# Performance work log

Measured on AMD Instinct MI355X. Metric: run time of the kernel, lower is better.

Reference implementation:

```python
import jax, jax.numpy as jnp
import numpy as np

DIM = 768
HEADS = 12
FRAMES = 16
T = FRAMES // 2          # temporal length per stream = 8
N = 196                  # spatial patch tokens (14x14)
B = 16                   # batch
SCALE = (DIM // HEADS) ** -0.5


def setup_inputs() -> dict:
    key = jax.random.key(0)
    ks = jax.random.split(key, 10)
    return {
        "s_x": jax.random.normal(ks[0], (N + 1, B * T, DIM), jnp.float32),
        "t_x": jax.random.normal(ks[1], (B, T * N, DIM), jnp.float32),
        "clip_time_pos": SCALE * jax.random.normal(ks[2], (T, DIM), jnp.float32),
        "vmae_time_pos": SCALE * jax.random.normal(ks[3], (T, DIM), jnp.float32),
        "Wq": jax.random.normal(ks[4], (DIM, DIM), jnp.float32) * 0.02,
        "q_bias": jnp.zeros((DIM,), jnp.float32),
        "Wkv": jax.random.normal(ks[5], (2 * DIM, DIM), jnp.float32) * 0.02,
        "kv_bias": jnp.zeros((2 * DIM,), jnp.float32),
        "Wproj": jax.random.normal(ks[6], (DIM, DIM), jnp.float32) * 0.02,
        "proj_bias": jnp.zeros((DIM,), jnp.float32),
    }


def reference(s_x, t_x, clip_time_pos, vmae_time_pos,
              Wq, q_bias, Wkv, kv_bias, Wproj, proj_bias):
    b = t_x.shape[0]
    t = s_x.shape[1] // b            # = FRAMES // 2
    n = s_x.shape[0] - 1             # spatial tokens (CLS excluded)
    d = s_x.shape[-1]
    h = HEADS
    hd = d // h
    scale = hd ** -0.5

    s_cls = s_x[0]                                   # [b*t, d]
    # 'n (b t) d -> (b n) t d'
    s_pat = s_x[1:].reshape(n, b, t, d).transpose(1, 0, 2, 3).reshape(b * n, t, d)
    s_pat = s_pat + clip_time_pos                    # [(b n), t, d]
    # 'b (t n) d -> (b n) t d'
    tx = t_x.reshape(b, t, n, d).transpose(0, 2, 1, 3).reshape(b * n, t, d)
    tx = tx + vmae_time_pos

    # projections (bias added manually as in F.linear with explicit bias)
    q = (s_pat @ Wq.T + q_bias).reshape(b * n, t, h, hd).transpose(0, 2, 1, 3)  # [bn,h,t,hd]
    kv = (tx @ Wkv.T + kv_bias).reshape(b * n, t, 2, h, hd)                      # e outermost in (e h d)
    k = kv[:, :, 0].transpose(0, 2, 1, 3)            # [bn,h,t,hd]
    v = kv[:, :, 1].transpose(0, 2, 1, 3)

    attn = jax.nn.softmax(jnp.einsum('bhqd,bhkd->bhqk', q * scale, k), axis=-1)
    out = jnp.einsum('bhqk,bhkd->bhqd', attn, v)     # [bn,h,t,hd]
    out = out.transpose(0, 2, 1, 3).reshape(b * n, t, d)
    out = out @ Wproj.T + proj_bias
    # '(b n) t d -> n (b t) d'
    out = out.reshape(b, n, t, d).transpose(1, 0, 2, 3).reshape(n, b * t, d)
    return jnp.concatenate([s_cls[None], out], axis=0)
```

## Files before the change

### kernel.cpp

```cpp
#include <hip/hip_runtime.h>
#include <stdint.h>

#define DIM   768
#define NTOK  196
#define TT    8
#define MROWS 25088
#define HEADS 12
#define NKT   12

typedef __bf16 bf16x8 __attribute__((ext_vector_type(8)));
typedef float  f32x4  __attribute__((ext_vector_type(4)));
typedef unsigned short u16x4 __attribute__((ext_vector_type(4)));
typedef unsigned short u16x8 __attribute__((ext_vector_type(8)));

typedef __attribute__((address_space(1))) const void GAS;
typedef __attribute__((address_space(3))) void LAS;

__device__ inline unsigned short f2bf(float f) {
  uint32_t u = __builtin_bit_cast(uint32_t, f);
  u += 0x7FFFu + ((u >> 16) & 1u);
  return (unsigned short)(u >> 16);
}
__device__ inline float bf2f(unsigned short s) {
  uint32_t u = ((uint32_t)s) << 16;
  return __builtin_bit_cast(float, u);
}
__device__ inline void gl_lds16(const unsigned short* g, unsigned short* l) {
  __builtin_amdgcn_global_load_lds((GAS*)g, (LAS*)l, 16, 0, 0);
}
__device__ inline int xcd_swz(int orig, int nwg) {
  int xcd = orig & 7, loc = orig >> 3;
  int q = nwg >> 3, r = nwg & 7;
  int base = (xcd < r) ? xcd * (q + 1) : r * (q + 1) + (xcd - r) * q;
  return base + loc;
}

#define WAITV(n) asm volatile("s_waitcnt vmcnt(" #n ")" ::: "memory")
#define CFENCE   asm volatile("" ::: "memory")

__global__ void wprep_kernel(const float* __restrict__ wq,
                             const float* __restrict__ wkv,
                             const float* __restrict__ wproj,
                             unsigned short* __restrict__ out) {
  int idx4 = blockIdx.x * blockDim.x + threadIdx.x;
  const int total4 = 2359296 / 4;
  if (idx4 >= total4) return;
  int e = idx4 * 4;
  const float* src; int off;
  if (e < 589824)        { src = wq;    off = e; }
  else if (e < 1769472)  { src = wkv;   off = e - 589824; }
  else                   { src = wproj; off = e - 1769472; }
  f32x4 v = *reinterpret_cast<const f32x4*>(&src[off]);
  u16x4 o;
  o[0] = f2bf(v[0]); o[1] = f2bf(v[1]); o[2] = f2bf(v[2]); o[3] = f2bf(v[3]);
  *reinterpret_cast<u16x4*>(&out[e]) = o;
}

__global__ void cls_kernel(const float* __restrict__ sx, float* __restrict__ out) {
  int i4 = blockIdx.x * blockDim.x + threadIdx.x;
  if (i4 < (128 * 768) / 4)
    reinterpret_cast<f32x4*>(out)[i4] = reinterpret_cast<const f32x4*>(sx)[i4];
}

__global__ __launch_bounds__(256)
void aprep2_kernel(const float* __restrict__ s_x, const float* __restrict__ t_x,
                   const float* __restrict__ clip, const float* __restrict__ vmae,
                   unsigned short* __restrict__ dstS, unsigned short* __restrict__ dstT,
                   int ybase) {
  int idx = blockIdx.x * blockDim.x + threadIdx.x;
  const int total = MROWS * (DIM / 8);
  if (idx >= total) return;
  int m  = idx / 96;
  int c8 = (idx - m * 96) * 8;
  int bn = m >> 3, t = m & 7;
  int b  = bn / NTOK, n = bn - b * NTOK;
  const float* src; const float* tp; unsigned short* dst; int srow;
  if ((int)blockIdx.y + ybase == 0) {
    srow = (1 + n) * 128 + b * 8 + t; src = s_x; tp = clip; dst = dstS;
  } else {
    srow = b * (TT * NTOK) + t * NTOK + n; src = t_x; tp = vmae; dst = dstT;
  }
  const float* sp = &src[srow * DIM + c8];
  const float* pp = &tp[t * DIM + c8];
  f32x4 a0 = reinterpret_cast<const f32x4*>(sp)[0];
  f32x4 a1 = reinterpret_cast<const f32x4*>(sp)[1];
  f32x4 p0 = reinterpret_cast<const f32x4*>(pp)[0];
  f32x4 p1 = reinterpret_cast<const f32x4*>(pp)[1];
  a0 += p0; a1 += p1;
  u16x8 o;
  o[0] = f2bf(a0[0]); o[1] = f2bf(a0[1]); o[2] = f2bf(a0[2]); o[3] = f2bf(a0[3]);
  o[4] = f2bf(a1[0]); o[5] = f2bf(a1[1]); o[6] = f2bf(a1[2]); o[7] = f2bf(a1[3]);
  *reinterpret_cast<u16x8*>(&dst[m * DIM + c8]) = o;
}

__global__ __launch_bounds__(512)
void gemm8(const unsigned short* __restrict__ As,
           const unsigned short* __restrict__ At,
           const unsigned short* __restrict__ W0,
           const unsigned short* __restrict__ W1,
           const float* __restrict__ b0,
           const float* __restrict__ b1,
           unsigned short* __restrict__ out0,
           unsigned short* __restrict__ out1,
           int bid0) {
  __shared__ unsigned short SB[3 * 24576];

  const int tid  = threadIdx.x;
  const int lane = tid & 63;
  const int w    = tid >> 6;
  const int wm   = w >> 2;
  const int wn   = w & 3;

  int bid = xcd_swz(blockIdx.x, gridDim.x) + bid0;

  const unsigned short *Ag, *Wg;
  const float* bias;
  unsigned short* ob;
  int rt, ct, Ncols;
  float scale = 1.0f;
  if (bid < 588) { rt = bid / 6;  ct = bid % 6;  Ag = As; Wg = W0; bias = b0; ob = out0; Ncols = 768;  scale = 0.125f; }
  else { int b2 = bid - 588; rt = b2 / 12; ct = b2 % 12; Ag = At; Wg = W1; bias = b1; ob = out1; Ncols = 1536; }
  const int m0 = rt * 256;
  const int n0 = ct * 128;

  auto stageA = [&](int kt) {
    const int kb = kt * 64;
    unsigned short* dst = &SB[(kt % 3) * 24576];
    #pragma unroll
    for (int rnd = 0; rnd < 4; ++rnd) {
      int s    = rnd * 8 + w;
      int srow = s * 8 + (lane >> 3);
      int scol = ((lane & 7) * 8) ^ ((srow & 7) << 3);
      gl_lds16(&Ag[(size_t)(m0 + srow) * 768 + kb + scol], dst + s * 512);
    }
  };
  auto stageB = [&](int kt) {
    const int kb = kt * 64;
    unsigned short* dst = &SB[(kt % 3) * 24576 + 16384];
    #pragma unroll
    for (int rnd = 0; rnd < 2; ++rnd) {
      int s    = rnd * 8 + w;
      int srow = s * 8 + (lane >> 3);
      int scol = ((lane & 7) * 8) ^ ((srow & 7) << 3);
      gl_lds16(&Wg[(size_t)(n0 + srow) * 768 + kb + scol], dst + s * 512);
    }
  };

  f32x4 acc[8][2] = {};

  stageA(0); stageB(0);
  stageA(1); stageB(1);

  for (int kt = 0; kt < NKT; ++kt) {
    __builtin_amdgcn_sched_barrier(0);
    if (kt < NKT - 1) { WAITV(6); } else { WAITV(0); }
    __builtin_amdgcn_s_barrier();
    CFENCE;

    const unsigned short* Ab = &SB[(kt % 3) * 24576];
    const unsigned short* Bb = Ab + 16384;
    const bool st = (kt + 2) < NKT;

    if (st) stageA(kt + 2);
    __builtin_amdgcn_sched_barrier(0);

    #pragma unroll
    for (int ks = 0; ks < 2; ++ks) {
      bf16x8 af[8], bfv[2];
      const int kc = ks * 32 + (lane >> 4) * 8;
      #pragma unroll
      for (int fm = 0; fm < 8; ++fm) {
        int r = wm * 128 + fm * 16 + (lane & 15);
        af[fm] = *reinterpret_cast<const bf16x8*>(&Ab[r * 64 + (kc ^ ((r & 7) << 3))]);
      }
      #pragma unroll
      for (int fn = 0; fn < 2; ++fn) {
        int r = wn * 32 + fn * 16 + (lane & 15);
        bfv[fn] = *reinterpret_cast<const bf16x8*>(&Bb[r * 64 + (kc ^ ((r & 7) << 3))]);
      }
      __builtin_amdgcn_s_setprio(1);
      #pragma unroll
      for (int fm = 0; fm < 8; ++fm)
        #pragma unroll
        for (int fn = 0; fn < 2; ++fn)
          acc[fm][fn] = __builtin_amdgcn_mfma_f32_16x16x32_bf16(af[fm], bfv[fn], acc[fm][fn], 0, 0, 0);
      __builtin_amdgcn_s_setprio(0);
      if (ks == 0 && st) stageB(kt + 2);
      __builtin_amdgcn_sched_barrier(0);
    }
  }

  #pragma unroll
  for (int fm = 0; fm < 8; ++fm) {
    #pragma unroll
    for (int fn = 0; fn < 2; ++fn) {
      int col = n0 + wn * 32 + fn * 16 + (lane & 15);
      float bsv = bias[col];
      #pragma unroll
      for (int i = 0; i < 4; ++i) {
        int row = m0 + wm * 128 + fm * 16 + (lane >> 4) * 4 + i;
        float v = (acc[fm][fn][i] + bsv) * scale;
        ob[(size_t)row * Ncols + col] = f2bf(v);
      }
    }
  }
}

__global__ __launch_bounds__(512)
void gemm_proj(const unsigned short* __restrict__ Ag,
               const unsigned short* __restrict__ Wg,
               const float* __restrict__ bias,
               float* __restrict__ fout) {
  __shared__ unsigned short SB[3 * 16384];

  const int tid  = threadIdx.x;
  const int lane = tid & 63;
  const int w    = tid >> 6;
  const int wm   = w >> 2, wn = w & 3;

  int bid = xcd_swz(blockIdx.x, gridDim.x);
  const int rt = bid / 6, ct = bid % 6;
  const int m0 = rt * 128, n0 = ct * 128;

  auto stageP = [&](int kt, const unsigned short* src, int base_row, int half) {
    const int kb = kt * 64;
    unsigned short* dst = &SB[(kt % 3) * 16384 + half * 8192];
    #pragma unroll
    for (int rnd = 0; rnd < 2; ++rnd) {
      int s    = rnd * 8 + w;
      int srow = s * 8 + (lane >> 3);
      int scol = ((lane & 7) * 8) ^ ((srow & 7) << 3);
      gl_lds16(&src[(size_t)(base_row + srow) * 768 + kb + scol], dst + s * 512);
    }
  };

  f32x4 acc[4][2] = {};

  stageP(0, Ag, m0, 0); stageP(0, Wg, n0, 1);
  stageP(1, Ag, m0, 0); stageP(1, Wg, n0, 1);

  for (int kt = 0; kt < NKT; ++kt) {
    __builtin_amdgcn_sched_barrier(0);
    if (kt < NKT - 1) { WAITV(4); } else { WAITV(0); }
    __builtin_amdgcn_s_barrier();
    CFENCE;

    const unsigned short* Ab = &SB[(kt % 3) * 16384];
    const unsigned short* Bb = Ab + 8192;
    const bool st = (kt + 2) < NKT;

    if (st) stageP(kt + 2, Ag, m0, 0);
    __builtin_amdgcn_sched_barrier(0);

    #pragma unroll
    for (int ks = 0; ks < 2; ++ks) {
      bf16x8 af[4], bfv[2];
      const int kc = ks * 32 + (lane >> 4) * 8;
      #pragma unroll
      for (int fm = 0; fm < 4; ++fm) {
        int r = wm * 64 + fm * 16 + (lane & 15);
        af[fm] = *reinterpret_cast<const bf16x8*>(&Ab[r * 64 + (kc ^ ((r & 7) << 3))]);
      }
      #pragma unroll
      for (int fn = 0; fn < 2; ++fn) {
        int r = wn * 32 + fn * 16 + (lane & 15);
        bfv[fn] = *reinterpret_cast<const bf16x8*>(&Bb[r * 64 + (kc ^ ((r & 7) << 3))]);
      }
      __builtin_amdgcn_s_setprio(1);
      #pragma unroll
      for (int fm = 0; fm < 4; ++fm)
        #pragma unroll
        for (int fn = 0; fn < 2; ++fn)
          acc[fm][fn] = __builtin_amdgcn_mfma_f32_16x16x32_bf16(af[fm], bfv[fn], acc[fm][fn], 0, 0, 0);
      __builtin_amdgcn_s_setprio(0);
      if (ks == 0 && st) stageP(kt + 2, Wg, n0, 1);
      __builtin_amdgcn_sched_barrier(0);
    }
  }

  #pragma unroll
  for (int fm = 0; fm < 4; ++fm) {
    #pragma unroll
    for (int fn = 0; fn < 2; ++fn) {
      int col = n0 + wn * 32 + fn * 16 + (lane & 15);
      float bsv = bias[col];
      #pragma unroll
      for (int i = 0; i < 4; ++i) {
        int row = m0 + wm * 64 + fm * 16 + (lane >> 4) * 4 + i;
        float v = acc[fm][fn][i] + bsv;
        int bn = row >> 3, t = row & 7;
        int b  = bn / NTOK, n = bn - b * NTOK;
        fout[((1 + n) * 128 + b * 8 + t) * DIM + col] = v;
      }
    }
  }
}

__global__ __launch_bounds__(256)
void attn_kernel(const unsigned short* __restrict__ qb,
                 const unsigned short* __restrict__ kvb,
                 unsigned short* __restrict__ ob) {
  __shared__ __align__(16) float lds[4][3][8][68];
  const int tid  = threadIdx.x;
  const int lane = tid & 63;
  const int w    = tid >> 6;
  const int wid  = blockIdx.x * 4 + w;
  const int bn   = wid / HEADS;
  const int h    = wid - bn * HEADS;

  const int t  = lane >> 3;
  const int d0 = (lane & 7) * 8;
  const int qoff = (bn * 8 + t) * DIM + h * 64 + d0;
  const int koff = (bn * 8 + t) * (2 * DIM) + h * 64 + d0;

  u16x8 q8 = *reinterpret_cast<const u16x8*>(&qb[qoff]);
  u16x8 k8 = *reinterpret_cast<const u16x8*>(&kvb[koff]);
  u16x8 v8 = *reinterpret_cast<const u16x8*>(&kvb[koff + DIM]);
  f32x4 qa, qc, ka, kc, va, vc;
  #pragma unroll
  for (int e = 0; e < 4; ++e) {
    qa[e] = bf2f(q8[e]); qc[e] = bf2f(q8[e + 4]);
    ka[e] = bf2f(k8[e]); kc[e] = bf2f(k8[e + 4]);
    va[e] = bf2f(v8[e]); vc[e] = bf2f(v8[e + 4]);
  }
  *reinterpret_cast<f32x4*>(&lds[w][0][t][d0])     = qa;
  *reinterpret_cast<f32x4*>(&lds[w][0][t][d0 + 4]) = qc;
  *reinterpret_cast<f32x4*>(&lds[w][1][t][d0])     = ka;
  *reinterpret_cast<f32x4*>(&lds[w][1][t][d0 + 4]) = kc;
  *reinterpret_cast<f32x4*>(&lds[w][2][t][d0])     = va;
  *reinterpret_cast<f32x4*>(&lds[w][2][t][d0 + 4]) = vc;
  __syncthreads();

  const int i = lane >> 3, j = lane & 7;
  const f32x4* qi = reinterpret_cast<const f32x4*>(&lds[w][0][i][0]);
  const f32x4* kj = reinterpret_cast<const f32x4*>(&lds[w][1][j][0]);
  float s = 0.f;
  #pragma unroll
  for (int c = 0; c < 16; ++c) {
    f32x4 a = qi[c], b = kj[c];
    s += a[0] * b[0] + a[1] * b[1] + a[2] * b[2] + a[3] * b[3];
  }
  float m = s;
  m = fmaxf(m, __shfl_xor(m, 1));
  m = fmaxf(m, __shfl_xor(m, 2));
  m = fmaxf(m, __shfl_xor(m, 4));
  float e = __expf(s - m);
  float sum = e;
  sum += __shfl_xor(sum, 1);
  sum += __shfl_xor(sum, 2);
  sum += __shfl_xor(sum, 4);
  float p = e / sum;

  float o[8] = {};
  #pragma unroll
  for (int jj = 0; jj < 8; ++jj) {
    float pj = __shfl(p, (lane & 56) | jj);
    const f32x4* vj = reinterpret_cast<const f32x4*>(&lds[w][2][jj][d0]);
    f32x4 v0 = vj[0], v1 = vj[1];
    o[0] += pj * v0[0]; o[1] += pj * v0[1]; o[2] += pj * v0[2]; o[3] += pj * v0[3];
    o[4] += pj * v1[0]; o[5] += pj * v1[1]; o[6] += pj * v1[2]; o[7] += pj * v1[3];
  }
  u16x8 os;
  #pragma unroll
  for (int e2 = 0; e2 < 8; ++e2) os[e2] = f2bf(o[e2]);
  *reinterpret_cast<u16x8*>(&ob[qoff]) = os;
}

extern "C" void kernel_launch(void* const* d_in, const int* in_sizes, int n_in,
                              void* d_out, int out_size, void* d_ws, size_t ws_size,
                              hipStream_t stream) {
  const float* s_x       = (const float*)d_in[0];
  const float* t_x       = (const float*)d_in[1];
  const float* clip_pos  = (const float*)d_in[2];
  const float* vmae_pos  = (const float*)d_in[3];
  const float* Wq        = (const float*)d_in[4];
  const float* q_bias    = (const float*)d_in[5];
  const float* Wkv       = (const float*)d_in[6];
  const float* kv_bias   = (const float*)d_in[7];
  const float* Wproj     = (const float*)d_in[8];
  const float* proj_bias = (const float*)d_in[9];
  float* out = (float*)d_out;

  char* ws = (char*)d_ws;
  unsigned short* w_bf = (unsigned short*)ws;
  const size_t ABUF = 38535168, KVB = 77070336, WB = 4718592;
  const bool merged = ws_size >= (WB + 3 * ABUF + KVB);

  const unsigned short* wq_bf  = w_bf;
  const unsigned short* wkv_bf = w_bf + 589824;
  const unsigned short* wpj_bf = w_bf + 1769472;

  const int prep_blocks = (MROWS * 96 + 255) / 256;

  wprep_kernel<<<dim3((589824 + 255) / 256), dim3(256), 0, stream>>>(Wq, Wkv, Wproj, w_bf);
  cls_kernel<<<dim3(96), dim3(256), 0, stream>>>(s_x, out);

  if (merged) {
    unsigned short* As    = (unsigned short*)(ws + WB);
    unsigned short* At    = (unsigned short*)(ws + WB + ABUF);
    unsigned short* q_bf  = (unsigned short*)(ws + WB + 2 * ABUF);
    unsigned short* kv_bf = (unsigned short*)(ws + WB + 3 * ABUF);
    aprep2_kernel<<<dim3(prep_blocks, 2), dim3(256), 0, stream>>>(
        s_x, t_x, clip_pos, vmae_pos, As, At, 0);
    gemm8<<<dim3(1764), dim3(512), 0, stream>>>(As, At, wq_bf, wkv_bf, q_bias, kv_bias,
                                                q_bf, kv_bf, 0);
    attn_kernel<<<dim3(9408), dim3(256), 0, stream>>>(q_bf, kv_bf, As);
    gemm_proj<<<dim3(1176), dim3(512), 0, stream>>>(As, wpj_bf, proj_bias, out);
  } else {
    unsigned short* buf1  = (unsigned short*)(ws + WB);
    unsigned short* q_bf  = (unsigned short*)(ws + WB + ABUF);
    unsigned short* kv_bf = (unsigned short*)(ws + WB + 2 * ABUF);
    aprep2_kernel<<<dim3(prep_blocks, 1), dim3(256), 0, stream>>>(
        s_x, t_x, clip_pos, vmae_pos, buf1, buf1, 0);
    gemm8<<<dim3(588), dim3(512), 0, stream>>>(buf1, buf1, wq_bf, wkv_bf, q_bias, kv_bias,
                                               q_bf, kv_bf, 0);
    aprep2_kernel<<<dim3(prep_blocks, 1), dim3(256), 0, stream>>>(
        s_x, t_x, clip_pos, vmae_pos, buf1, buf1, 1);
    gemm8<<<dim3(1176), dim3(512), 0, stream>>>(buf1, buf1, wq_bf, wkv_bf, q_bias, kv_bias,
                                                q_bf, kv_bf, 588);
    attn_kernel<<<dim3(9408), dim3(256), 0, stream>>>(q_bf, kv_bf, buf1);
    gemm_proj<<<dim3(1176), dim3(512), 0, stream>>>(buf1, wpj_bf, proj_bias, out);
  }
}
```

Baseline: 210.5 us.

## Reshape GEMM warp tiling to 64x64 per wave and batch LDS fragment loads

The QKV GEMM warp layout changes from 128x32 per wave to 64x64 per wave, which balances A and B fragment reuse and cuts the number of LDS reads per MFMA. In both GEMMs, all fragments for the two k-substeps are now loaded up front and the MFMAs are issued in one block. The staging of the next A and B tiles is also moved together ahead of the compute, removing the interleaved sched_barriers. This raises register pressure from holding more fragments and gives the compiler more freedom over scheduling, which could hurt overlap.

```diff
diff --git a/kernel.cpp b/kernel.cpp
--- a/kernel.cpp
+++ b/kernel.cpp
@@ -108,8 +108,8 @@
   const int tid  = threadIdx.x;
   const int lane = tid & 63;
   const int w    = tid >> 6;
-  const int wm   = w >> 2;
-  const int wn   = w & 3;
+  const int wm   = w & 3;
+  const int wn   = w >> 2;
 
   int bid = xcd_swz(blockIdx.x, gridDim.x) + bid0;
 
@@ -146,7 +146,7 @@
     }
   };
 
-  f32x4 acc[8][2] = {};
+  f32x4 acc[4][4] = {};
 
   stageA(0); stageB(0);
   stageA(1); stageB(1);
@@ -161,44 +161,44 @@
     const unsigned short* Bb = Ab + 16384;
     const bool st = (kt + 2) < NKT;
 
-    if (st) stageA(kt + 2);
+    if (st) { stageA(kt + 2); stageB(kt + 2); }
     __builtin_amdgcn_sched_barrier(0);
 
+    bf16x8 af[2][4], bfv[2][4];
     #pragma unroll
     for (int ks = 0; ks < 2; ++ks) {
-      bf16x8 af[8], bfv[2];
       const int kc = ks * 32 + (lane >> 4) * 8;
       #pragma unroll
-      for (int fm = 0; fm < 8; ++fm) {
-        int r = wm * 128 + fm * 16 + (lane & 15);
-        af[fm] = *reinterpret_cast<const bf16x8*>(&Ab[r * 64 + (kc ^ ((r & 7) << 3))]);
-      }
-      #pragma unroll
-      for (int fn = 0; fn < 2; ++fn) {
-        int r = wn * 32 + fn * 16 + (lane & 15);
-        bfv[fn] = *reinterpret_cast<const bf16x8*>(&Bb[r * 64 + (kc ^ ((r & 7) << 3))]);
-      }
-      __builtin_amdgcn_s_setprio(1);
-      #pragma unroll
-      for (int fm = 0; fm < 8; ++fm)
+      for (int fm = 0; fm < 4; ++fm) {
+        int r = wm * 64 + fm * 16 + (lane & 15);
+        af[ks][fm] = *reinterpret_cast<const bf16x8*>(&Ab[r * 64 + (kc ^ ((r & 7) << 3))]);
+      }
+      #pragma unroll
+      for (int fn = 0; fn < 4; ++fn) {
+        int r = wn * 64 + fn * 16 + (lane & 15);
+        bfv[ks][fn] = *reinterpret_cast<const bf16x8*>(&Bb[r * 64 + (kc ^ ((r & 7) << 3))]);
+      }
+    }
+    __builtin_amdgcn_s_setprio(1);
+    #pragma unroll
+    for (int ks = 0; ks < 2; ++ks)
+      #pragma unroll
+      for (int fm = 0; fm < 4; ++fm)
         #pragma unroll
-        for (int fn = 0; fn < 2; ++fn)
-          acc[fm][fn] = __builtin_amdgcn_mfma_f32_16x16x32_bf16(af[fm], bfv[fn], acc[fm][fn], 0, 0, 0);
-      __builtin_amdgcn_s_setprio(0);
-      if (ks == 0 && st) stageB(kt + 2);
-      __builtin_amdgcn_sched_barrier(0);
-    }
-  }
-
-  #pragma unroll
-  for (int fm = 0; fm < 8; ++fm) {
-    #pragma unroll
-    for (int fn = 0; fn < 2; ++fn) {
-      int col = n0 + wn * 32 + fn * 16 + (lane & 15);
+        for (int fn = 0; fn < 4; ++fn)
+          acc[fm][fn] = __builtin_amdgcn_mfma_f32_16x16x32_bf16(af[ks][fm], bfv[ks][fn], acc[fm][fn], 0, 0, 0);
+    __builtin_amdgcn_s_setprio(0);
+  }
+
+  #pragma unroll
+  for (int fm = 0; fm < 4; ++fm) {
+    #pragma unroll
+    for (int fn = 0; fn < 4; ++fn) {
+      int col = n0 + wn * 64 + fn * 16 + (lane & 15);
       float bsv = bias[col];
       #pragma unroll
       for (int i = 0; i < 4; ++i) {
-        int row = m0 + wm * 128 + fm * 16 + (lane >> 4) * 4 + i;
+        int row = m0 + wm * 64 + fm * 16 + (lane >> 4) * 4 + i;
         float v = (acc[fm][fn][i] + bsv) * scale;
         ob[(size_t)row * Ncols + col] = f2bf(v);
       }
@@ -249,33 +249,33 @@
     const unsigned short* Bb = Ab + 8192;
     const bool st = (kt + 2) < NKT;
 
-    if (st) stageP(kt + 2, Ag, m0, 0);
+    if (st) { stageP(kt + 2, Ag, m0, 0); stageP(kt + 2, Wg, n0, 1); }
     __builtin_amdgcn_sched_barrier(0);
 
+    bf16x8 af[2][4], bfv[2][2];
     #pragma unroll
     for (int ks = 0; ks < 2; ++ks) {
-      bf16x8 af[4], bfv[2];
       const int kc = ks * 32 + (lane >> 4) * 8;
       #pragma unroll
       for (int fm = 0; fm < 4; ++fm) {
         int r = wm * 64 + fm * 16 + (lane & 15);
-        af[fm] = *reinterpret_cast<const bf16x8*>(&Ab[r * 64 + (kc ^ ((r & 7) << 3))]);
+        af[ks][fm] = *reinterpret_cast<const bf16x8*>(&Ab[r * 64 + (kc ^ ((r & 7) << 3))]);
       }
       #pragma unroll
       for (int fn = 0; fn < 2; ++fn) {
         int r = wn * 32 + fn * 16 + (lane & 15);
-        bfv[fn] = *reinterpret_cast<const bf16x8*>(&Bb[r * 64 + (kc ^ ((r & 7) << 3))]);
-      }
-      __builtin_amdgcn_s_setprio(1);
+        bfv[ks][fn] = *reinterpret_cast<const bf16x8*>(&Bb[r * 64 + (kc ^ ((r & 7) << 3))]);
+      }
+    }
+    __builtin_amdgcn_s_setprio(1);
+    #pragma unroll
+    for (int ks = 0; ks < 2; ++ks)
       #pragma unroll
       for (int fm = 0; fm < 4; ++fm)
         #pragma unroll
         for (int fn = 0; fn < 2; ++fn)
-          acc[fm][fn] = __builtin_amdgcn_mfma_f32_16x16x32_bf16(af[fm], bfv[fn], acc[fm][fn], 0, 0, 0);
-      __builtin_amdgcn_s_setprio(0);
-      if (ks == 0 && st) stageP(kt + 2, Wg, n0, 1);
-      __builtin_amdgcn_sched_barrier(0);
-    }
+          acc[fm][fn] = __builtin_amdgcn_mfma_f32_16x16x32_bf16(af[ks][fm], bfv[ks][fn], acc[fm][fn], 0, 0, 0);
+    __builtin_amdgcn_s_setprio(0);
   }
 
   #pragma unroll
```

Measured after the change: 213.4 us. No clear change (+1.4%).
